# Kernel tuning notes

Measured on AMD Instinct MI355X. Metric: run time of the kernel, lower is better.

The kernel has to match this reference:

```python
import jax, jax.numpy as jnp
import numpy as np

N = 50000   # nodes
E = 800000  # edges
G = 64      # graphs in batch
H1, D1 = 2, 64   # gat1: 2 heads x 64
D2 = 32          # gat2: 1 head x 32
IN = 1
EPS = 1e-5


def _gat(h, src, dst, W, al, ar, Wres, bias, Hh, D):
    # DGL GATConv (eval mode): project, per-edge attention, edge softmax over dst, scatter-sum, residual + bias
    feat = (h @ W).reshape(N, Hh, D)                     # [N,H,D]
    el = jnp.sum(feat * al, axis=-1)                     # [N,H]
    er = jnp.sum(feat * ar, axis=-1)                     # [N,H]
    e = jax.nn.leaky_relu(el[src] + er[dst], 0.2)        # [E,H]
    m = jax.ops.segment_max(e, dst, num_segments=N)      # [N,H] (stable softmax)
    a = jnp.exp(e - m[dst])
    s = jax.ops.segment_sum(a, dst, num_segments=N)
    alpha = a / s[dst]                                   # [E,H]
    msg = feat[src] * alpha[:, :, None]                  # [E,H,D]
    rst = jax.ops.segment_sum(msg, dst, num_segments=N)  # [N,H,D]
    res = (h @ Wres).reshape(N, Hh, D)
    return rst + res + bias.reshape(1, Hh, D)


def _bn(x, gamma, beta, mean, var):
    return (x - mean) * jax.lax.rsqrt(var + EPS) * gamma + beta


def setup_inputs() -> dict:
    key = jax.random.key(0)
    ks = jax.random.split(key, 32)
    rn = lambda i, shape: jax.random.normal(ks[i], shape, jnp.float32) * 0.1
    inp = {
        'feat': jax.random.normal(ks[0], (N, IN), jnp.float32),
        'W1': rn(1, (IN, H1 * D1)), 'al1': rn(2, (H1, D1)), 'ar1': rn(3, (H1, D1)),
        'res1': rn(4, (IN, H1 * D1)), 'b1': rn(5, (H1 * D1,)),
        'g1_gamma': jnp.ones((H1 * D1,), jnp.float32), 'g1_beta': jnp.zeros((H1 * D1,), jnp.float32),
        'g1_mean': rn(6, (H1 * D1,)), 'g1_var': jax.random.uniform(ks[7], (H1 * D1,), jnp.float32) + 0.5,
        'W2': rn(8, (H1 * D1, D2)), 'al2': rn(9, (1, D2)), 'ar2': rn(10, (1, D2)),
        'res2': rn(11, (H1 * D1, D2)), 'b2': rn(12, (D2,)),
        'g2_gamma': jnp.ones((D2,), jnp.float32), 'g2_beta': jnp.zeros((D2,), jnp.float32),
        'g2_mean': rn(13, (D2,)), 'g2_var': jax.random.uniform(ks[14], (D2,), jnp.float32) + 0.5,
        'Wd1': rn(15, (D2, H1 * D1)), 'bd1': rn(16, (H1 * D1,)),
        'gd_gamma': jnp.ones((H1 * D1,), jnp.float32), 'gd_beta': jnp.zeros((H1 * D1,), jnp.float32),
        'gd_mean': rn(17, (H1 * D1,)), 'gd_var': jax.random.uniform(ks[18], (H1 * D1,), jnp.float32) + 0.5,
        'Wd2': rn(19, (H1 * D1, IN)), 'bd2': rn(20, (IN,)),
        'src': jax.random.randint(ks[21], (E,), 0, N, jnp.int32),
        'dst': jax.random.randint(ks[22], (E,), 0, N, jnp.int32),
        'graph_ids': jnp.sort(jax.random.randint(ks[23], (N,), 0, G, jnp.int32)),
    }
    return inp


def reference(feat, W1, al1, ar1, res1, b1, g1_gamma, g1_beta, g1_mean, g1_var,
              W2, al2, ar2, res2, b2, g2_gamma, g2_beta, g2_mean, g2_var,
              Wd1, bd1, gd_gamma, gd_beta, gd_mean, gd_var, Wd2, bd2,
              src, dst, graph_ids):
    h = _gat(feat, src, dst, W1, al1, ar1, res1, b1, H1, D1)   # [N,2,64]
    h = h.reshape(N, H1 * D1)
    h = jax.nn.relu(_bn(h, g1_gamma, g1_beta, g1_mean, g1_var))
    h = _gat(h, src, dst, W2, al2, ar2, res2, b2, 1, D2)       # [N,1,32]
    h = h.reshape(N, D2)
    h = jax.nn.relu(_bn(h, g2_gamma, g2_beta, g2_mean, g2_var))
    # dgl.mean_nodes over batched graphs
    counts = jax.ops.segment_sum(jnp.ones((N,), h.dtype), graph_ids, num_segments=G)
    graph_rep = jax.ops.segment_sum(h, graph_ids, num_segments=G) / jnp.maximum(counts, 1.0)[:, None]
    # decoder: Linear -> BN -> ReLU -> Linear (dropout off in eval)
    d = jax.nn.relu(_bn(h @ Wd1 + bd1, gd_gamma, gd_beta, gd_mean, gd_var))
    reconstruction = d @ Wd2 + bd2
    return graph_rep, reconstruction
```

## Files before the change

### kernel.cpp

```cpp
#include <hip/hip_runtime.h>
#include <hip/hip_bf16.h>
#include <hip/hip_fp16.h>

#define NN 50000
#define NE 800000
#define NG 64
#define C1 128
#define D2 32
#define CAP 32
#define RNG 6250
#define NCH 391
#define BN_EPS 1e-5f

#define CST_A   0
#define CST_B   2
#define CST_P   4
#define CST_Q   132
#define CST_R   260
#define CST_SC2 388
#define CST_RC2 420
#define CST_SD  452
#define CST_RD  580
#define CST_N   1024

#define UO_DEGP  0
#define UO_OVFC  800000
#define ZERO_UNITS 800004
#define UO_FLAG  800004
#define UO_CST   800008
#define UO_ESRC2 801040
#define UO_OVF   1601040
#define UO_FCAN  3201040
#define UO_F2    3251040
#define UO_RS2   4051040
#define UO_EL2   5651040
#define UO_ER2   5701040
#define UO_END   5751040

typedef _Float16 h2vec __attribute__((ext_vector_type(2)));

__device__ __forceinline__ float lrelu(float x) { return fmaxf(x, 0.2f * x); }
__device__ __forceinline__ float bu2f(unsigned int u) {
    union { unsigned int i; float f; } v; v.i = (u & 0xFFFFu) << 16; return v.f;
}
__device__ __forceinline__ unsigned short f2bu(float f) {
    union { float f; unsigned int i; } v; v.f = f;
    unsigned int r = v.i + 0x7FFFu + ((v.i >> 16) & 1u);
    return (unsigned short)(r >> 16);
}
__device__ __forceinline__ unsigned int packh2(float a, float b) {
    h2vec h; h.x = (_Float16)a; h.y = (_Float16)b;
    union { h2vec h; unsigned int u; } v; v.h = h; return v.u;
}
__device__ __forceinline__ h2vec as_h2(unsigned int u) {
    union { unsigned int u; h2vec h; } v; v.u = u; return v.h;
}
__device__ __forceinline__ float ldw(const void* p, int i, int bf) {
    return bf ? bu2f(((const unsigned short*)p)[i]) : ((const float*)p)[i];
}
__device__ __forceinline__ int sniff64(const unsigned int* fw, int l) {
    int cnt = 0;
    for (int j = l; j < 256; j += 64) {
        unsigned int b = (fw[j] >> 8) & 0x7Fu;
        cnt += (b >= 0x3Au && b <= 0x41u) ? 1 : 0;
    }
#pragma unroll
    for (int m = 32; m >= 1; m >>= 1) cnt += __shfl_xor(cnt, m);
    return (cnt > 128) ? 1 : 0;
}

__global__ void k_prep(const void* __restrict__ feat, const int* __restrict__ dst,
                       const int* __restrict__ src,
                       float* __restrict__ fcan, int* __restrict__ degp,
                       unsigned short* __restrict__ esrc2,
                       int2* __restrict__ ovf, int* __restrict__ ovfc,
                       const void* W1, const void* al1, const void* ar1,
                       const void* res1, const void* b1,
                       const void* g1g, const void* g1b, const void* g1m, const void* g1v,
                       const void* b2v, const void* g2g, const void* g2b,
                       const void* g2m, const void* g2v,
                       const void* bd1, const void* gdg, const void* gdb,
                       const void* gdm, const void* gdv,
                       int* __restrict__ flag, float* __restrict__ cst) {
    __shared__ int sBf;
    int t = threadIdx.x;
    if (t < 64) {
        int bf = sniff64((const unsigned int*)feat, t);
        if (t == 0) sBf = bf;
    }
    __syncthreads();
    int bf = sBf;
    int r = blockIdx.x / NCH;
    int c = blockIdx.x % NCH;

    if (blockIdx.x == 0) {
        if (t == 0) *flag = bf;
        if (t < 128) {
            if (t < 2) {
                float a = 0.0f, b = 0.0f;
                for (int d = 0; d < 64; ++d) {
                    float w = ldw(W1, t * 64 + d, bf);
                    a += w * ldw(al1, t * 64 + d, bf);
                    b += w * ldw(ar1, t * 64 + d, bf);
                }
                cst[CST_A + t] = a;
                cst[CST_B + t] = b;
            }
            {
                float sc = rsqrtf(ldw(g1v, t, bf) + BN_EPS) * ldw(g1g, t, bf);
                cst[CST_P + t] = ldw(W1, t, bf) * sc;
                cst[CST_Q + t] = ldw(res1, t, bf) * sc;
                cst[CST_R + t] = (ldw(b1, t, bf) - ldw(g1m, t, bf)) * sc + ldw(g1b, t, bf);
            }
            if (t < D2) {
                float sc = rsqrtf(ldw(g2v, t, bf) + BN_EPS) * ldw(g2g, t, bf);
                cst[CST_SC2 + t] = sc;
                cst[CST_RC2 + t] = (ldw(b2v, t, bf) - ldw(g2m, t, bf)) * sc + ldw(g2b, t, bf);
            }
            {
                float sc = rsqrtf(ldw(gdv, t, bf) + BN_EPS) * ldw(gdg, t, bf);
                cst[CST_SD + t] = sc;
                cst[CST_RD + t] = (ldw(bd1, t, bf) - ldw(gdm, t, bf)) * sc + ldw(gdb, t, bf);
            }
        }
    }

    int lo = r * RNG, hi = lo + RNG;
#pragma unroll
    for (int j = 0; j < 8; ++j) {
        int k = c * 2048 + j * 256 + t;
        if (k < NE) {
            int d = dst[k];
            if (d >= lo && d < hi) {
                int slot = atomicAdd(&degp[d << 4], 1);
                if (slot < CAP) {
                    esrc2[d * CAP + slot] = (unsigned short)src[k];
                } else {
                    int p = atomicAdd(ovfc, 1);
                    ovf[p] = make_int2(d, src[k]);
                }
            }
        }
        if (r == 0 && k < NN) fcan[k] = ldw(feat, k, bf);
    }
}

__global__ __launch_bounds__(256) void k_layer1(
        const float* __restrict__ fcan, const void* W2, const void* res2,
        const void* al2, const void* ar2,
        const int* __restrict__ flag, const float* __restrict__ cst,
        const int* __restrict__ degp, const unsigned short* __restrict__ esrc2,
        const int2* __restrict__ ovf, const int* __restrict__ ovfc,
        unsigned short* __restrict__ F2, float* __restrict__ RS2,
        float* __restrict__ EL2, float* __restrict__ ER2) {
    __shared__ unsigned int sW2pk[32 * 66];
    __shared__ unsigned int sR2pk[32 * 66];
    __shared__ unsigned int sH1pk[32 * 66];
    __shared__ float sP[C1], sQ[C1], sR[C1];
    __shared__ float sAl[D2], sAr[D2];
    int t = threadIdx.x;
    int bf = *flag;
    for (int u = t; u < 2048; u += 256) {
        int cw = u >> 5, l2 = u & 31;
        sW2pk[l2 * 66 + cw] = packh2(ldw(W2, cw * D2 + l2, bf),
                                     ldw(W2, (cw + 64) * D2 + l2, bf));
        sR2pk[l2 * 66 + cw] = packh2(ldw(res2, cw * D2 + l2, bf),
                                     ldw(res2, (cw + 64) * D2 + l2, bf));
    }
    if (t < C1) { sP[t] = cst[CST_P + t]; sQ[t] = cst[CST_Q + t]; sR[t] = cst[CST_R + t]; }
    if (t < D2) { sAl[t] = ldw(al2, t, bf); sAr[t] = ldw(ar2, t, bf); }
    __syncthreads();

    int l = t & 31;
    int g = t >> 5;
    int base = blockIdx.x * 32;
    float A0 = cst[CST_A + 0], A1 = cst[CST_A + 1];
    float B0 = cst[CST_B + 0], B1 = cst[CST_B + 1];

    int dcap[4], draw[4];
    float fiK[4];
#pragma unroll
    for (int k = 0; k < 4; ++k) {
        int i = base + g * 4 + k;
        if (i < NN) {
            draw[k] = degp[i << 4];
            dcap[k] = draw[k] < CAP ? draw[k] : CAP;
            fiK[k] = fcan[i];
        } else { draw[k] = 0; dcap[k] = 0; fiK[k] = 0.0f; }
    }
    float S0[4], S1[4], N0[4], N1[4];
#pragma unroll
    for (int k = 0; k < 4; ++k) { S0[k] = S1[k] = N0[k] = N1[k] = 0.0f; }
    int sA[4];
#pragma unroll
    for (int k = 0; k < 4; ++k)
        sA[k] = (l < dcap[k]) ? (int)esrc2[(base + g * 4 + k) * CAP + l] : 0;
    float fA[4];
#pragma unroll
    for (int k = 0; k < 4; ++k) fA[k] = fcan[sA[k]];
#pragma unroll
    for (int k = 0; k < 4; ++k) {
        if (l < dcap[k]) {
            float w0 = __expf(lrelu(A0 * fA[k] + B0 * fiK[k]));
            float w1 = __expf(lrelu(A1 * fA[k] + B1 * fiK[k]));
            S0[k] += w0; N0[k] += w0 * fA[k];
            S1[k] += w1; N1[k] += w1 * fA[k];
        }
    }
#pragma unroll
    for (int k = 0; k < 4; ++k) {
        if (draw[k] > CAP) {
            int i = base + g * 4 + k;
            int novf = *ovfc;
            for (int p = l; p < novf; p += 32) {
                int2 o = ovf[p];
                if (o.x == i) {
                    float fs = fcan[o.y];
                    float w0 = __expf(lrelu(A0 * fs + B0 * fiK[k]));
                    float w1 = __expf(lrelu(A1 * fs + B1 * fiK[k]));
                    S0[k] += w0; N0[k] += w0 * fs;
                    S1[k] += w1; N1[k] += w1 * fs;
                }
            }
        }
    }
#pragma unroll
    for (int m = 16; m >= 1; m >>= 1) {
#pragma unroll
        for (int k = 0; k < 4; ++k) {
            S0[k] += __shfl_xor(S0[k], m); N0[k] += __shfl_xor(N0[k], m);
            S1[k] += __shfl_xor(S1[k], m); N1[k] += __shfl_xor(N1[k], m);
        }
    }
#pragma unroll
    for (int k = 0; k < 4; ++k) {
        int slot = g * 4 + k;
        float T0 = S0[k] > 0.0f ? N0[k] / S0[k] : 0.0f;
        float T1 = S1[k] > 0.0f ? N1[k] / S1[k] : 0.0f;
        float h0  = fmaxf(sP[l]      * T0 + sQ[l]      * fiK[k] + sR[l],      0.0f);
        float h1v = fmaxf(sP[l + 32] * T0 + sQ[l + 32] * fiK[k] + sR[l + 32], 0.0f);
        float h2v = fmaxf(sP[l + 64] * T1 + sQ[l + 64] * fiK[k] + sR[l + 64], 0.0f);
        float h3v = fmaxf(sP[l + 96] * T1 + sQ[l + 96] * fiK[k] + sR[l + 96], 0.0f);
        sH1pk[slot * 66 + l]      = packh2(h0,  h2v);
        sH1pk[slot * 66 + l + 32] = packh2(h1v, h3v);
    }
    __syncthreads();

    int w = t >> 6;
    int half = (t >> 5) & 1;
    int nb0 = w * 8 + half * 4;
    float aF[4] = {0.f, 0.f, 0.f, 0.f}, aR[4] = {0.f, 0.f, 0.f, 0.f};
    for (int cw = 0; cw < 64; cw += 2) {
        uint2 wq = *(const uint2*)&sW2pk[l * 66 + cw];
        uint2 rq = *(const uint2*)&sR2pk[l * 66 + cw];
#pragma unroll
        for (int n = 0; n < 4; ++n) {
            uint2 hq = *(const uint2*)&sH1pk[(nb0 + n) * 66 + cw];
            aF[n] = __builtin_amdgcn_fdot2(as_h2(hq.x), as_h2(wq.x),
                    __builtin_amdgcn_fdot2(as_h2(hq.y), as_h2(wq.y), aF[n], false), false);
            aR[n] = __builtin_amdgcn_fdot2(as_h2(hq.x), as_h2(rq.x),
                    __builtin_amdgcn_fdot2(as_h2(hq.y), as_h2(rq.y), aR[n], false), false);
        }
    }
#pragma unroll
    for (int n = 0; n < 4; ++n) {
        int i = base + nb0 + n;
        if (i < NN) {
            float elp = aF[n] * sAl[l], erp = aF[n] * sAr[l];
#pragma unroll
            for (int m = 16; m >= 1; m >>= 1) {
                elp += __shfl_xor(elp, m);
                erp += __shfl_xor(erp, m);
            }
            if (l == 0) { EL2[i] = elp; ER2[i] = erp; }
            F2[(size_t)i * D2 + l]  = f2bu(aF[n]);
            RS2[(size_t)i * D2 + l] = aR[n];
        }
    }
}

__global__ __launch_bounds__(256) void k_final(
        const void* Wd1, const void* Wd2, const void* bd2,
        const int* __restrict__ flag, const float* __restrict__ cst,
        const int* __restrict__ degp, const unsigned short* __restrict__ esrc2,
        const int2* __restrict__ ovf, const int* __restrict__ ovfc,
        const unsigned short* __restrict__ F2, float* __restrict__ RS2,
        const float* __restrict__ EL2, const float* __restrict__ ER2,
        float* __restrict__ out) {
    __shared__ float sWd1[C1 * D2];
    __shared__ float sWd2[C1];
    __shared__ float sSd[C1], sRd[C1];
    __shared__ float sSc2[D2], sRc2[D2];
    __shared__ float sH2[8 * D2];
    __shared__ unsigned int sWS[8 * 64];
    int t = threadIdx.x;
    int bf = *flag;
    for (int u = t; u < C1 * D2; u += 256) sWd1[u] = ldw(Wd1, u, bf);
    for (int u = t; u < C1; u += 256) {
        sWd2[u] = ldw(Wd2, u, bf);
        sSd[u] = cst[CST_SD + u]; sRd[u] = cst[CST_RD + u];
    }
    if (t < D2) { sSc2[t] = cst[CST_SC2 + t]; sRc2[t] = cst[CST_RC2 + t]; }
    __syncthreads();

    int i = (blockIdx.x * 256 + t) >> 5;
    int l = t & 31;
    int nb = t >> 5;

    float eri = ER2[i];
    int dr = degp[i << 4];
    int dcap = dr < CAP ? dr : CAP;
    const unsigned short* row = &esrc2[i * CAP];

    int sMy = 0; float wMy = 0.0f;
    if (l < dcap) {
        sMy = (int)row[l];
        wMy = __expf(lrelu(EL2[sMy] + eri));
    }
    float S = wMy;
#pragma unroll
    for (int m = 16; m >= 1; m >>= 1) S += __shfl_xor(S, m);
    sWS[nb * 64 + 2 * l]     = __float_as_uint(wMy);
    sWS[nb * 64 + 2 * l + 1] = (unsigned int)sMy;

    float aF0 = 0.f, aF1 = 0.f, aF2 = 0.f, aF3 = 0.f;
    int e = 0;
    for (; e + 3 < dcap; e += 4) {
        uint2 p0 = *(const uint2*)&sWS[nb * 64 + 2 * e];
        uint2 p1 = *(const uint2*)&sWS[nb * 64 + 2 * (e + 1)];
        uint2 p2 = *(const uint2*)&sWS[nb * 64 + 2 * (e + 2)];
        uint2 p3 = *(const uint2*)&sWS[nb * 64 + 2 * (e + 3)];
        float v0 = bu2f(F2[(size_t)p0.y * D2 + l]);
        float v1 = bu2f(F2[(size_t)p1.y * D2 + l]);
        float v2 = bu2f(F2[(size_t)p2.y * D2 + l]);
        float v3 = bu2f(F2[(size_t)p3.y * D2 + l]);
        aF0 = fmaf(__uint_as_float(p0.x), v0, aF0);
        aF1 = fmaf(__uint_as_float(p1.x), v1, aF1);
        aF2 = fmaf(__uint_as_float(p2.x), v2, aF2);
        aF3 = fmaf(__uint_as_float(p3.x), v3, aF3);
    }
    for (; e < dcap; ++e) {
        uint2 p = *(const uint2*)&sWS[nb * 64 + 2 * e];
        aF0 = fmaf(__uint_as_float(p.x), bu2f(F2[(size_t)p.y * D2 + l]), aF0);
    }
    if (dr > CAP) {
        int novf = *ovfc;
        for (int p = 0; p < novf; ++p) {
            int2 o = ovf[p];
            if (o.x == i) {
                float wA = __expf(lrelu(EL2[o.y] + eri));
                S += wA;
                aF0 = fmaf(wA, bu2f(F2[(size_t)o.y * D2 + l]), aF0);
            }
        }
    }
    float aF = (aF0 + aF1) + (aF2 + aF3);
    float inv = S > 0.0f ? 1.0f / S : 0.0f;

    float h2 = fmaxf((aF * inv + RS2[(size_t)i * D2 + l]) * sSc2[l] + sRc2[l], 0.0f);
    RS2[(size_t)i * D2 + l] = h2;

    sH2[nb * D2 + l] = h2;
    float ac0 = 0.0f, ac1 = 0.0f, ac2 = 0.0f, ac3 = 0.0f;
#pragma unroll
    for (int d = 0; d < D2; ++d) {
        float h = sH2[nb * D2 + d];
        const float* wr = &sWd1[d * C1 + l];
        ac0 = fmaf(h, wr[0],  ac0);
        ac1 = fmaf(h, wr[32], ac1);
        ac2 = fmaf(h, wr[64], ac2);
        ac3 = fmaf(h, wr[96], ac3);
    }
    float rec = fmaxf(ac0 * sSd[l]      + sRd[l],      0.0f) * sWd2[l]
              + fmaxf(ac1 * sSd[l + 32] + sRd[l + 32], 0.0f) * sWd2[l + 32]
              + fmaxf(ac2 * sSd[l + 64] + sRd[l + 64], 0.0f) * sWd2[l + 64]
              + fmaxf(ac3 * sSd[l + 96] + sRd[l + 96], 0.0f) * sWd2[l + 96];
#pragma unroll
    for (int m = 16; m >= 1; m >>= 1) rec += __shfl_xor(rec, m);
    if (l == 0) out[NG * D2 + i] = rec + ldw(bd2, 0, bf);
}

__global__ __launch_bounds__(256) void k_pool2(const int* __restrict__ gid,
                                               const float* __restrict__ H2,
                                               float* __restrict__ out) {
    __shared__ int sLo, sHi;
    __shared__ float sAcc[32 * 32];
    int g = blockIdx.x;
    int t = threadIdx.x;
    if (t == 0) {
        int lo = 0, hi = NN;
        while (lo < hi) { int m = (lo + hi) >> 1; if (gid[m] < g) lo = m + 1; else hi = m; }
        sLo = lo;
        lo = 0; hi = NN;
        while (lo < hi) { int m = (lo + hi) >> 1; if (gid[m] < g + 1) lo = m + 1; else hi = m; }
        sHi = lo;
    }
    __syncthreads();
    int lo = sLo, hi = sHi;
    int q = t & 7;
    int row = t >> 3;
    float4 acc = make_float4(0.f, 0.f, 0.f, 0.f);
    for (int i = lo + row; i < hi; i += 32) {
        float4 v = ((const float4*)&H2[(size_t)i * D2])[q];
        acc.x += v.x; acc.y += v.y; acc.z += v.z; acc.w += v.w;
    }
    *(float4*)&sAcc[row * 32 + 4 * q] = acc;
    __syncthreads();
    if (t < 32) {
        float a = 0.0f;
        for (int r = 0; r < 32; ++r) a += sAcc[r * 32 + t];
        float c = (float)(hi - lo);
        out[g * D2 + t] = a / fmaxf(c, 1.0f);
    }
}

extern "C" void kernel_launch(void* const* d_in, const int* in_sizes, int n_in,
                              void* d_out, int out_size, void* d_ws, size_t ws_size,
                              hipStream_t stream) {
    const void* feat = d_in[0];
    const void* W1 = d_in[1];  const void* al1 = d_in[2];  const void* ar1 = d_in[3];
    const void* res1 = d_in[4]; const void* b1 = d_in[5];
    const void* g1g = d_in[6]; const void* g1b = d_in[7];
    const void* g1m = d_in[8]; const void* g1v = d_in[9];
    const void* W2 = d_in[10]; const void* al2 = d_in[11]; const void* ar2 = d_in[12];
    const void* res2 = d_in[13]; const void* b2v = d_in[14];
    const void* g2g = d_in[15]; const void* g2b = d_in[16];
    const void* g2m = d_in[17]; const void* g2v = d_in[18];
    const void* Wd1 = d_in[19]; const void* bd1 = d_in[20];
    const void* gdg = d_in[21]; const void* gdb = d_in[22];
    const void* gdm = d_in[23]; const void* gdv = d_in[24];
    const void* Wd2 = d_in[25]; const void* bd2 = d_in[26];
    const int* src = (const int*)d_in[27];
    const int* dst = (const int*)d_in[28];
    const int* gid = (const int*)d_in[29];

    unsigned int* wsu = (unsigned int*)d_ws;
    int* degp   = (int*)(wsu + UO_DEGP);
    int* ovfc   = (int*)(wsu + UO_OVFC);
    int* flag   = (int*)(wsu + UO_FLAG);
    float* cst  = (float*)(wsu + UO_CST);
    unsigned short* esrc2 = (unsigned short*)(wsu + UO_ESRC2);
    int2* ovf   = (int2*)(wsu + UO_OVF);
    float* fcan = (float*)(wsu + UO_FCAN);
    unsigned short* F2 = (unsigned short*)(wsu + UO_F2);
    float* RS2  = (float*)(wsu + UO_RS2);
    float* EL2  = (float*)(wsu + UO_EL2);
    float* ER2  = (float*)(wsu + UO_ER2);

    hipMemsetAsync(d_ws, 0, (size_t)ZERO_UNITS * 4, stream);

    k_prep<<<NCH * 8, 256, 0, stream>>>(feat, dst, src, fcan, degp,
                                        esrc2, ovf, ovfc,
                                        W1, al1, ar1, res1, b1,
                                        g1g, g1b, g1m, g1v,
                                        b2v, g2g, g2b, g2m, g2v,
                                        bd1, gdg, gdb, gdm, gdv,
                                        flag, cst);

    k_layer1<<<(NN + 31) / 32, 256, 0, stream>>>(fcan, W2, res2, al2, ar2, flag, cst,
                                                 degp, esrc2, ovf, ovfc,
                                                 F2, RS2, EL2, ER2);

    k_final<<<(NN * 32) / 256, 256, 0, stream>>>(Wd1, Wd2, bd2, flag, cst,
                                                 degp, esrc2, ovf, ovfc,
                                                 F2, RS2, EL2, ER2,
                                                 (float*)d_out);

    k_pool2<<<NG, 256, 0, stream>>>(gid, RS2, (float*)d_out);
}
```

Measured before the change: 245.6 us.

## Make edge bucketing XCC-aware with work-stealing, slim decoder LDS, split pooling

The edge-bucketing prep kernel becomes a persistent kernel. Each block reads its XCC id and first claims chunks of its own destination range through per-range atomic work counters, so a range's degree/slot atomics tend to stay within one XCC's L2. The final kernel drops most shared arrays and keeps BN constants and Wd2 in registers. It broadcasts h2 with shuffles instead of an LDS round trip, reads Wd1 as a float4-interleaved LDS layout, and raises occupancy via launch bounds. Graph mean pooling is split across four blocks per graph with atomic accumulation into a zeroed output, which adds a memset and makes float summation order nondeterministic.

```diff
diff --git a/kernel.cpp b/kernel.cpp
--- a/kernel.cpp
+++ b/kernel.cpp
@@ -11,6 +11,7 @@
 #define RNG 6250
 #define NCH 391
 #define BN_EPS 1e-5f
+#define PREP_BLOCKS 2048
 
 #define CST_A   0
 #define CST_B   2
@@ -25,17 +26,18 @@
 
 #define UO_DEGP  0
 #define UO_OVFC  800000
-#define ZERO_UNITS 800004
-#define UO_FLAG  800004
-#define UO_CST   800008
-#define UO_ESRC2 801040
-#define UO_OVF   1601040
-#define UO_FCAN  3201040
-#define UO_F2    3251040
-#define UO_RS2   4051040
-#define UO_EL2   5651040
-#define UO_ER2   5701040
-#define UO_END   5751040
+#define UO_WK    800016
+#define ZERO_UNITS 800144
+#define UO_FLAG  800144
+#define UO_CST   800160
+#define UO_ESRC2 801184
+#define UO_OVF   1601184
+#define UO_FCAN  3201184
+#define UO_F2    3251184
+#define UO_RS2   4051184
+#define UO_EL2   5651184
+#define UO_ER2   5701184
+#define UO_END   5751184
 
 typedef _Float16 h2vec __attribute__((ext_vector_type(2)));
 
@@ -69,11 +71,13 @@
     return (cnt > 128) ? 1 : 0;
 }
 
-__global__ void k_prep(const void* __restrict__ feat, const int* __restrict__ dst,
+__global__ __launch_bounds__(256) void k_prep(
+                       const void* __restrict__ feat, const int* __restrict__ dst,
                        const int* __restrict__ src,
                        float* __restrict__ fcan, int* __restrict__ degp,
                        unsigned short* __restrict__ esrc2,
                        int2* __restrict__ ovf, int* __restrict__ ovfc,
+                       int* __restrict__ wk,
                        const void* W1, const void* al1, const void* ar1,
                        const void* res1, const void* b1,
                        const void* g1g, const void* g1b, const void* g1m, const void* g1v,
@@ -83,15 +87,14 @@
                        const void* gdm, const void* gdv,
                        int* __restrict__ flag, float* __restrict__ cst) {
     __shared__ int sBf;
+    __shared__ int sC;
     int t = threadIdx.x;
     if (t < 64) {
-        int bf = sniff64((const unsigned int*)feat, t);
-        if (t == 0) sBf = bf;
+        int b = sniff64((const unsigned int*)feat, t);
+        if (t == 0) sBf = b;
     }
     __syncthreads();
     int bf = sBf;
-    int r = blockIdx.x / NCH;
-    int c = blockIdx.x % NCH;
 
     if (blockIdx.x == 0) {
         if (t == 0) *flag = bf;
@@ -125,23 +128,39 @@
         }
     }
 
-    int lo = r * RNG, hi = lo + RNG;
-#pragma unroll
-    for (int j = 0; j < 8; ++j) {
-        int k = c * 2048 + j * 256 + t;
-        if (k < NE) {
-            int d = dst[k];
-            if (d >= lo && d < hi) {
-                int slot = atomicAdd(&degp[d << 4], 1);
-                if (slot < CAP) {
-                    esrc2[d * CAP + slot] = (unsigned short)src[k];
-                } else {
-                    int p = atomicAdd(ovfc, 1);
-                    ovf[p] = make_int2(d, src[k]);
+    for (int k = blockIdx.x * 256 + t; k < NN; k += PREP_BLOCKS * 256)
+        fcan[k] = ldw(feat, k, bf);
+
+    int xcc;
+    asm volatile("s_getreg_b32 %0, hwreg(HW_REG_XCC_ID)" : "=s"(xcc));
+    xcc &= 7;
+
+    for (int rr = 0; rr < 8; ++rr) {
+        int r = (xcc + rr) & 7;
+        int lo = r * RNG, hi = lo + RNG;
+        for (;;) {
+            if (t == 0) sC = atomicAdd(&wk[r * 16], 1);
+            __syncthreads();
+            int c = sC;
+            __syncthreads();
+            if (c >= NCH) break;
+#pragma unroll
+            for (int j = 0; j < 8; ++j) {
+                int k = c * 2048 + j * 256 + t;
+                if (k < NE) {
+                    int d = dst[k];
+                    if (d >= lo && d < hi) {
+                        int slot = atomicAdd(&degp[d << 4], 1);
+                        if (slot < CAP) {
+                            esrc2[d * CAP + slot] = (unsigned short)src[k];
+                        } else {
+                            int p = atomicAdd(ovfc, 1);
+                            ovf[p] = make_int2(d, src[k]);
+                        }
+                    }
                 }
             }
         }
-        if (r == 0 && k < NN) fcan[k] = ldw(feat, k, bf);
     }
 }
 
@@ -279,7 +298,7 @@
     }
 }
 
-__global__ __launch_bounds__(256) void k_final(
+__global__ __launch_bounds__(256, 8) void k_final(
         const void* Wd1, const void* Wd2, const void* bd2,
         const int* __restrict__ flag, const float* __restrict__ cst,
         const int* __restrict__ degp, const unsigned short* __restrict__ esrc2,
@@ -287,25 +306,27 @@
         const unsigned short* __restrict__ F2, float* __restrict__ RS2,
         const float* __restrict__ EL2, const float* __restrict__ ER2,
         float* __restrict__ out) {
-    __shared__ float sWd1[C1 * D2];
-    __shared__ float sWd2[C1];
-    __shared__ float sSd[C1], sRd[C1];
-    __shared__ float sSc2[D2], sRc2[D2];
-    __shared__ float sH2[8 * D2];
+    __shared__ float sWd1x[4096];
     __shared__ unsigned int sWS[8 * 64];
     int t = threadIdx.x;
     int bf = *flag;
-    for (int u = t; u < C1 * D2; u += 256) sWd1[u] = ldw(Wd1, u, bf);
-    for (int u = t; u < C1; u += 256) {
-        sWd2[u] = ldw(Wd2, u, bf);
-        sSd[u] = cst[CST_SD + u]; sRd[u] = cst[CST_RD + u];
-    }
-    if (t < D2) { sSc2[t] = cst[CST_SC2 + t]; sRc2[t] = cst[CST_RC2 + t]; }
-    __syncthreads();
+    for (int u = t; u < 4096; u += 256) {
+        int d = u >> 7, lq = (u >> 2) & 31, j = u & 3;
+        sWd1x[u] = ldw(Wd1, d * C1 + j * 32 + lq, bf);
+    }
 
     int i = (blockIdx.x * 256 + t) >> 5;
     int l = t & 31;
     int nb = t >> 5;
+
+    float sc2 = cst[CST_SC2 + l], rc2 = cst[CST_RC2 + l];
+    float sd0 = cst[CST_SD + l],      rd0 = cst[CST_RD + l];
+    float sd1 = cst[CST_SD + l + 32], rd1 = cst[CST_RD + l + 32];
+    float sd2 = cst[CST_SD + l + 64], rd2 = cst[CST_RD + l + 64];
+    float sd3 = cst[CST_SD + l + 96], rd3 = cst[CST_RD + l + 96];
+    float wd2_0 = ldw(Wd2, l, bf),      wd2_1 = ldw(Wd2, l + 32, bf);
+    float wd2_2 = ldw(Wd2, l + 64, bf), wd2_3 = ldw(Wd2, l + 96, bf);
+    __syncthreads();
 
     float eri = ER2[i];
     int dr = degp[i << 4];
@@ -357,24 +378,24 @@
     float aF = (aF0 + aF1) + (aF2 + aF3);
     float inv = S > 0.0f ? 1.0f / S : 0.0f;
 
-    float h2 = fmaxf((aF * inv + RS2[(size_t)i * D2 + l]) * sSc2[l] + sRc2[l], 0.0f);
+    float h2 = fmaxf((aF * inv + RS2[(size_t)i * D2 + l]) * sc2 + rc2, 0.0f);
     RS2[(size_t)i * D2 + l] = h2;
 
-    sH2[nb * D2 + l] = h2;
+    const float4* Wx = (const float4*)sWd1x;
     float ac0 = 0.0f, ac1 = 0.0f, ac2 = 0.0f, ac3 = 0.0f;
 #pragma unroll
     for (int d = 0; d < D2; ++d) {
-        float h = sH2[nb * D2 + d];
-        const float* wr = &sWd1[d * C1 + l];
-        ac0 = fmaf(h, wr[0],  ac0);
-        ac1 = fmaf(h, wr[32], ac1);
-        ac2 = fmaf(h, wr[64], ac2);
-        ac3 = fmaf(h, wr[96], ac3);
-    }
-    float rec = fmaxf(ac0 * sSd[l]      + sRd[l],      0.0f) * sWd2[l]
-              + fmaxf(ac1 * sSd[l + 32] + sRd[l + 32], 0.0f) * sWd2[l + 32]
-              + fmaxf(ac2 * sSd[l + 64] + sRd[l + 64], 0.0f) * sWd2[l + 64]
-              + fmaxf(ac3 * sSd[l + 96] + sRd[l + 96], 0.0f) * sWd2[l + 96];
+        float h = __shfl(h2, d, 32);
+        float4 wv = Wx[d * 32 + l];
+        ac0 = fmaf(h, wv.x, ac0);
+        ac1 = fmaf(h, wv.y, ac1);
+        ac2 = fmaf(h, wv.z, ac2);
+        ac3 = fmaf(h, wv.w, ac3);
+    }
+    float rec = fmaxf(ac0 * sd0 + rd0, 0.0f) * wd2_0
+              + fmaxf(ac1 * sd1 + rd1, 0.0f) * wd2_1
+              + fmaxf(ac2 * sd2 + rd2, 0.0f) * wd2_2
+              + fmaxf(ac3 * sd3 + rd3, 0.0f) * wd2_3;
 #pragma unroll
     for (int m = 16; m >= 1; m >>= 1) rec += __shfl_xor(rec, m);
     if (l == 0) out[NG * D2 + i] = rec + ldw(bd2, 0, bf);
@@ -385,7 +406,8 @@
                                                float* __restrict__ out) {
     __shared__ int sLo, sHi;
     __shared__ float sAcc[32 * 32];
-    int g = blockIdx.x;
+    int g = blockIdx.x >> 2;
+    int part = blockIdx.x & 3;
     int t = threadIdx.x;
     if (t == 0) {
         int lo = 0, hi = NN;
@@ -400,7 +422,7 @@
     int q = t & 7;
     int row = t >> 3;
     float4 acc = make_float4(0.f, 0.f, 0.f, 0.f);
-    for (int i = lo + row; i < hi; i += 32) {
+    for (int i = lo + part * 32 + row; i < hi; i += 128) {
         float4 v = ((const float4*)&H2[(size_t)i * D2])[q];
         acc.x += v.x; acc.y += v.y; acc.z += v.z; acc.w += v.w;
     }
@@ -409,8 +431,8 @@
     if (t < 32) {
         float a = 0.0f;
         for (int r = 0; r < 32; ++r) a += sAcc[r * 32 + t];
-        float c = (float)(hi - lo);
-        out[g * D2 + t] = a / fmaxf(c, 1.0f);
+        float inv = 1.0f / fmaxf((float)(hi - lo), 1.0f);
+        atomicAdd(&out[g * D2 + t], a * inv);
     }
 }
 
@@ -437,6 +459,7 @@
     unsigned int* wsu = (unsigned int*)d_ws;
     int* degp   = (int*)(wsu + UO_DEGP);
     int* ovfc   = (int*)(wsu + UO_OVFC);
+    int* wk     = (int*)(wsu + UO_WK);
     int* flag   = (int*)(wsu + UO_FLAG);
     float* cst  = (float*)(wsu + UO_CST);
     unsigned short* esrc2 = (unsigned short*)(wsu + UO_ESRC2);
@@ -448,14 +471,15 @@
     float* ER2  = (float*)(wsu + UO_ER2);
 
     hipMemsetAsync(d_ws, 0, (size_t)ZERO_UNITS * 4, stream);
-
-    k_prep<<<NCH * 8, 256, 0, stream>>>(feat, dst, src, fcan, degp,
-                                        esrc2, ovf, ovfc,
-                                        W1, al1, ar1, res1, b1,
-                                        g1g, g1b, g1m, g1v,
-                                        b2v, g2g, g2b, g2m, g2v,
-                                        bd1, gdg, gdb, gdm, gdv,
-                                        flag, cst);
+    hipMemsetAsync(d_out, 0, (size_t)NG * D2 * sizeof(float), stream);
+
+    k_prep<<<PREP_BLOCKS, 256, 0, stream>>>(feat, dst, src, fcan, degp,
+                                            esrc2, ovf, ovfc, wk,
+                                            W1, al1, ar1, res1, b1,
+                                            g1g, g1b, g1m, g1v,
+                                            b2v, g2g, g2b, g2m, g2v,
+                                            bd1, gdg, gdb, gdm, gdv,
+                                            flag, cst);
 
     k_layer1<<<(NN + 31) / 32, 256, 0, stream>>>(fcan, W2, res2, al2, ar2, flag, cst,
                                                  degp, esrc2, ovf, ovfc,
@@ -466,5 +490,5 @@
                                                  F2, RS2, EL2, ER2,
                                                  (float*)d_out);
 
-    k_pool2<<<NG, 256, 0, stream>>>(gid, RS2, (float*)d_out);
-}
+    k_pool2<<<NG * 4, 256, 0, stream>>>(gid, RS2, (float*)d_out);
+}
```

After: 284.3 us. 15.8% more time.
